# Performance work log

Measured on AMD Instinct MI355X. Metric: run time of the kernel, lower is better.

Reference implementation:

```python
import jax, jax.numpy as jnp
import numpy as np

N, D = 512, 64          # n_objects, object_dim
HG, OG = 256, 256       # g hidden, g output
HF, OF = 256, 64        # f hidden, f output


def setup_inputs() -> dict:
    key = jax.random.key(0)
    ks = jax.random.split(key, 16)
    s = 0.05
    inp = {
        "x": jax.random.normal(ks[0], (N, D), dtype=jnp.float32),
        "q": jax.random.normal(ks[1], (D,), dtype=jnp.float32),
        # MLP g: input 3*D -> HG -> OG (ReLU after every layer, nonlinear=True)
        "g_w1": jax.random.normal(ks[2], (3 * D, HG), dtype=jnp.float32) * s,
        "g_b1": jnp.zeros((HG,), dtype=jnp.float32),
        "g_w2": jax.random.normal(ks[3], (HG, OG), dtype=jnp.float32) * s,
        "g_b2": jnp.zeros((OG,), dtype=jnp.float32),
        # query_expand: D -> HG -> OG (nonlinear=True)
        "qe_w1": jax.random.normal(ks[4], (D, HG), dtype=jnp.float32) * s,
        "qe_b1": jnp.zeros((HG,), dtype=jnp.float32),
        "qe_w2": jax.random.normal(ks[5], (HG, OG), dtype=jnp.float32) * s,
        "qe_b2": jnp.zeros((OG,), dtype=jnp.float32),
        # MLP f: OG -> HF -> OF (ReLU on hidden only, nonlinear=False)
        "f_w1": jax.random.normal(ks[6], (OG, HF), dtype=jnp.float32) * s,
        "f_b1": jnp.zeros((HF,), dtype=jnp.float32),
        "f_w2": jax.random.normal(ks[7], (HF, OF), dtype=jnp.float32) * s,
        "f_b2": jnp.zeros((OF,), dtype=jnp.float32),
    }
    return inp


def reference(x, q, g_w1, g_b1, g_w2, g_b2, qe_w1, qe_b1, qe_w2, qe_b2,
              f_w1, f_b1, f_w2, f_b2):
    n, d = x.shape
    # pair (a,b): first half x_i = x[b], second half x_j = x[a], then query q
    xi = jnp.broadcast_to(x[None, :, :], (n, n, d))   # repeats x along dim 0
    xj = jnp.broadcast_to(x[:, None, :], (n, n, d))   # repeats x along dim 1
    qb = jnp.broadcast_to(q[None, None, :], (n, n, d))
    pair_concat = jnp.concatenate([xi, xj, qb], axis=-1).reshape(n * n, 3 * d)
    # g MLP (ReLU after every layer since nonlinear=True)
    h = jax.nn.relu(pair_concat @ g_w1 + g_b1)
    relations = jax.nn.relu(h @ g_w2 + g_b2)          # [N*N, OG]
    # attentional weighting
    qh = jax.nn.relu(q @ qe_w1 + qe_b1)
    q_exp = jax.nn.relu(qh @ qe_w2 + qe_b2)           # [OG]
    c = jax.nn.softmax(relations @ q_exp, axis=0)     # [N*N]
    embedding = jnp.sum(relations * c[:, None], axis=0)  # [OG]
    # f MLP (no final nonlinearity)
    fh = jax.nn.relu(embedding @ f_w1 + f_b1)
    out = fh @ f_w2 + f_b2                            # [OF]
    return out
```

## Files before the change

kernel.cpp:

```cpp
#include <hip/hip_runtime.h>
#include <hip/hip_bf16.h>

typedef __attribute__((ext_vector_type(8))) short s16x8;
typedef __attribute__((ext_vector_type(4))) float f32x4;

#define NSLOT 128

__device__ __forceinline__ short f2bf(float f) {
    union { float f; unsigned u; } c; c.f = f;
    unsigned u = c.u;
    return (short)((u + 0x7fffu + ((u >> 16) & 1u)) >> 16);
}

__global__ __launch_bounds__(256) void rn_k1(
    const float* __restrict__ x, const float* __restrict__ q,
    const float* __restrict__ g_w1, const float* __restrict__ g_b1,
    const float* __restrict__ g_w2,
    const float* __restrict__ qe_w1, const float* __restrict__ qe_b1,
    const float* __restrict__ qe_w2, const float* __restrict__ qe_b2,
    float* __restrict__ U, float* __restrict__ V,
    float* __restrict__ c0, float* __restrict__ qexp,
    short* __restrict__ w2s, float* __restrict__ accb)
{
    const int blk = blockIdx.x, t = threadIdx.x;

    if (blk < 64) {
        __shared__ float xs[1024];
        const int rg = blk >> 1, half = blk & 1;
        const int r0 = rg << 4;
        #pragma unroll
        for (int i = 0; i < 4; ++i) {
            int idx = i * 256 + t;
            xs[idx] = x[(r0 << 6) + idx];
        }
        float w[64];
        #pragma unroll
        for (int k = 0; k < 64; ++k)
            w[k] = g_w1[(half * 64 + k) * 256 + t];
        __syncthreads();
        float* dst = half ? V : U;
        #pragma unroll 2
        for (int r = 0; r < 16; ++r) {
            float a0 = 0.f, a1 = 0.f, a2 = 0.f, a3 = 0.f;
            #pragma unroll
            for (int k = 0; k < 64; k += 4) {
                const float4 xv = *(const float4*)&xs[r * 64 + k];
                a0 += xv.x * w[k + 0];
                a1 += xv.y * w[k + 1];
                a2 += xv.z * w[k + 2];
                a3 += xv.w * w[k + 3];
            }
            dst[(r0 + r) * 256 + t] = (a0 + a1) + (a2 + a3);
        }
    } else if (blk == 64) {
        __shared__ float sbuf[64];
        __shared__ float qh[256];
        if (t < 64) sbuf[t] = q[t];
        __syncthreads();
        float cc = g_b1[t], hh = qe_b1[t];
        #pragma unroll 4
        for (int k = 0; k < 64; ++k) {
            float qv = sbuf[k];
            cc += qv * g_w1[(128 + k) * 256 + t];
            hh += qv * qe_w1[k * 256 + t];
        }
        c0[t] = cc;
        qh[t] = fmaxf(hh, 0.f);
        __syncthreads();
        float qe = qe_b2[t];
        #pragma unroll 4
        for (int k = 0; k < 256; ++k) qe += qh[k] * qe_w2[k * 256 + t];
        qexp[t] = fmaxf(qe, 0.f);
    } else if (blk < 97) {
        const int S0 = (blk - 65) * 2048 + t * 8;
        const float4 wA = *(const float4*)&g_w2[S0];
        const float4 wB = *(const float4*)&g_w2[S0 + 4];
        float wv8[8] = {wA.x, wA.y, wA.z, wA.w, wB.x, wB.y, wB.z, wB.w};
        #pragma unroll
        for (int i = 0; i < 8; ++i) {
            const int S = S0 + i;
            const int k = S >> 8, col = S & 255;
            const int wv = col >> 6, n = (col >> 4) & 3, l15 = col & 15;
            const int kk = k >> 5, g = (k >> 3) & 3, e = k & 7;
            const int lane = g * 16 + l15;
            w2s[((((wv * 8 + kk) * 4 + n) * 64 + lane) << 3) + e] = f2bf(wv8[i]);
        }
    } else {
        const int total = NSLOT * 257;
        int off = (blk - 97) * 2048 + t * 8;
        #pragma unroll
        for (int i = 0; i < 8; ++i)
            if (off + i < total) accb[off + i] = 0.f;
    }
}

__global__ __launch_bounds__(256, 4) void rn_k2(
    const float* __restrict__ U, const float* __restrict__ V,
    const float* __restrict__ c0, const float* __restrict__ qexp,
    const short* __restrict__ w2s, const float* __restrict__ g_b2,
    float* __restrict__ accb)
{
    __shared__ short hT[64][264];
    __shared__ float srowT[64][4];

    const int bid = blockIdx.x;
    const int a   = bid >> 3;
    const int b0  = (bid & 7) << 6;
    const int tid = threadIdx.x;
    const int wave = tid >> 6, lane = tid & 63;
    const int l15 = lane & 15, g = lane >> 4;
    const int col0 = wave << 6;

    {
        const int c4 = tid & 63;
        const int r0 = tid >> 6;
        const float4 vv  = *(const float4*)&V[a * 256 + c4 * 4];
        const float4 cc  = *(const float4*)&c0[c4 * 4];
        const float4 vcv = make_float4(vv.x + cc.x, vv.y + cc.y,
                                       vv.z + cc.z, vv.w + cc.w);
        #pragma unroll
        for (int it = 0; it < 16; ++it) {
            int row = r0 + it * 4;
            float4 uu = *(const float4*)&U[(b0 + row) * 256 + c4 * 4];
            __hip_bfloat162 p0 = __float22bfloat162_rn(
                make_float2(fmaxf(uu.x + vcv.x, 0.f), fmaxf(uu.y + vcv.y, 0.f)));
            __hip_bfloat162 p1 = __float22bfloat162_rn(
                make_float2(fmaxf(uu.z + vcv.z, 0.f), fmaxf(uu.w + vcv.w, 0.f)));
            uint2 st;
            st.x = *reinterpret_cast<unsigned*>(&p0);
            st.y = *reinterpret_cast<unsigned*>(&p1);
            *reinterpret_cast<uint2*>(&hT[row][c4 * 4]) = st;
        }
    }

    float qe[4], b2c[4];
    #pragma unroll
    for (int n = 0; n < 4; ++n) {
        int col = col0 + n * 16 + l15;
        qe[n]  = qexp[col];
        b2c[n] = g_b2[col];
    }
    __syncthreads();

    f32x4 acc[4][4];
    #pragma unroll
    for (int m = 0; m < 4; ++m)
        #pragma unroll
        for (int n = 0; n < 4; ++n)
            acc[m][n] = (f32x4){b2c[n], b2c[n], b2c[n], b2c[n]};

    #pragma unroll
    for (int kk = 0; kk < 8; ++kk) {
        const int koff = kk * 32 + g * 8;
        s16x8 bfr[4];
        #pragma unroll
        for (int n = 0; n < 4; ++n)
            bfr[n] = *(const s16x8*)&w2s[((wave << 14) + (((kk * 4 + n) << 9))) + (lane << 3)];
        s16x8 afr[4];
        #pragma unroll
        for (int m = 0; m < 4; ++m)
            afr[m] = *(const s16x8*)&hT[m * 16 + l15][koff];
        #pragma unroll
        for (int m = 0; m < 4; ++m)
            #pragma unroll
            for (int n = 0; n < 4; ++n)
                acc[m][n] = __builtin_amdgcn_mfma_f32_16x16x32_bf16(
                    afr[m], bfr[n], acc[m][n], 0, 0, 0);
    }

    #pragma unroll
    for (int m = 0; m < 4; ++m)
        #pragma unroll
        for (int n = 0; n < 4; ++n)
            #pragma unroll
            for (int j = 0; j < 4; ++j)
                acc[m][n][j] = fmaxf(acc[m][n][j], 0.f);

    #pragma unroll
    for (int m = 0; m < 4; ++m) {
        #pragma unroll
        for (int j = 0; j < 4; ++j) {
            float sp = 0.f;
            #pragma unroll
            for (int n = 0; n < 4; ++n) sp += acc[m][n][j] * qe[n];
            sp += __shfl_xor(sp, 1);
            sp += __shfl_xor(sp, 2);
            sp += __shfl_xor(sp, 4);
            sp += __shfl_xor(sp, 8);
            if (l15 == 0) srowT[m * 16 + g * 4 + j][wave] = sp;
        }
    }
    __syncthreads();

    float wrow[4][4];
    #pragma unroll
    for (int m = 0; m < 4; ++m)
        #pragma unroll
        for (int j = 0; j < 4; ++j) {
            const float4 s4 = *(const float4*)&srowT[m * 16 + g * 4 + j][0];
            wrow[m][j] = __expf(s4.x + s4.y + s4.z + s4.w);
        }

    const int slot = bid & (NSLOT - 1);
    if (wave == 0) {
        float ls = 0.f;
        #pragma unroll
        for (int m = 0; m < 4; ++m)
            #pragma unroll
            for (int j = 0; j < 4; ++j) ls += wrow[m][j];
        ls += __shfl_xor(ls, 16);
        ls += __shfl_xor(ls, 32);
        if (lane == 0) atomicAdd(&accb[slot * 257 + 256], ls);
    }

    #pragma unroll
    for (int n = 0; n < 4; ++n) {
        float wv = 0.f;
        #pragma unroll
        for (int m = 0; m < 4; ++m)
            #pragma unroll
            for (int j = 0; j < 4; ++j)
                wv += wrow[m][j] * acc[m][n][j];
        wv += __shfl_xor(wv, 16);
        wv += __shfl_xor(wv, 32);
        if (lane < 16) atomicAdd(&accb[slot * 257 + col0 + n * 16 + lane], wv);
    }
}

__global__ __launch_bounds__(1024) void rn_k4(
    const float* __restrict__ accb,
    const float* __restrict__ f_w1, const float* __restrict__ f_b1,
    const float* __restrict__ f_w2, const float* __restrict__ f_b2,
    float* __restrict__ out)
{
    __shared__ float part[4][256];
    __shared__ float emb[256];
    __shared__ float fh[256];
    __shared__ float lsa[128];
    const int t   = threadIdx.x;
    const int col = t & 255;
    const int sl  = t >> 8;

    float v = 0.f;
    #pragma unroll 8
    for (int s = sl; s < NSLOT; s += 4) v += accb[s * 257 + col];
    part[sl][col] = v;
    if (t < 128) lsa[t] = accb[t * 257 + 256];
    __syncthreads();

    if (sl == 0) {
        float ls = 0.f;
        #pragma unroll 8
        for (int s = 0; s < 128; ++s) ls += lsa[s];
        emb[col] = (part[0][col] + part[1][col] + part[2][col] + part[3][col]) / ls;
    }
    __syncthreads();

    {
        float h = 0.f;
        const int k0 = sl << 6;
        #pragma unroll 8
        for (int k = 0; k < 64; ++k)
            h += emb[k0 + k] * f_w1[(k0 + k) * 256 + col];
        part[sl][col] = h;
    }
    __syncthreads();
    if (sl == 0)
        fh[col] = fmaxf(part[0][col] + part[1][col] + part[2][col] + part[3][col]
                        + f_b1[col], 0.f);
    __syncthreads();

    if (t < 256) {
        const int oc = t & 63, ks = t >> 6;
        float o = 0.f;
        const int k0 = ks << 6;
        #pragma unroll 8
        for (int k = 0; k < 64; ++k)
            o += fh[k0 + k] * f_w2[(k0 + k) * 64 + oc];
        part[ks][oc] = o;
    }
    __syncthreads();
    if (t < 64)
        out[t] = part[0][t] + part[1][t] + part[2][t] + part[3][t] + f_b2[t];
}

extern "C" void kernel_launch(void* const* d_in, const int* in_sizes, int n_in,
                              void* d_out, int out_size, void* d_ws, size_t ws_size,
                              hipStream_t stream) {
    const float* x     = (const float*)d_in[0];
    const float* q     = (const float*)d_in[1];
    const float* g_w1  = (const float*)d_in[2];
    const float* g_b1  = (const float*)d_in[3];
    const float* g_w2  = (const float*)d_in[4];
    const float* g_b2  = (const float*)d_in[5];
    const float* qe_w1 = (const float*)d_in[6];
    const float* qe_b1 = (const float*)d_in[7];
    const float* qe_w2 = (const float*)d_in[8];
    const float* qe_b2 = (const float*)d_in[9];
    const float* f_w1  = (const float*)d_in[10];
    const float* f_b1  = (const float*)d_in[11];
    const float* f_w2  = (const float*)d_in[12];
    const float* f_b2  = (const float*)d_in[13];

    float* wsf  = (float*)d_ws;
    float* U    = wsf;
    float* V    = wsf + 131072;
    float* c0   = wsf + 262144;
    float* qexp = wsf + 262400;
    short* w2s  = (short*)(wsf + 262656);
    float* accb = wsf + 295424;

    hipLaunchKernelGGL(rn_k1, dim3(114), dim3(256), 0, stream,
                       x, q, g_w1, g_b1, g_w2, qe_w1, qe_b1, qe_w2, qe_b2,
                       U, V, c0, qexp, w2s, accb);
    hipLaunchKernelGGL(rn_k2, dim3(4096), dim3(256), 0, stream,
                       U, V, c0, qexp, (const short*)w2s, g_b2, accb);
    hipLaunchKernelGGL(rn_k4, dim3(1), dim3(1024), 0, stream,
                       accb, f_w1, f_b1, f_w2, f_b2, (float*)d_out);
}
```

Baseline: 72.59 us.

## Process four row tiles per block in rn_k2 with persistent loop

rn_k2 now launches 1024 blocks, and each block loops over four 64-row tiles instead of handling a single tile. The loop reuses the V+c0 vector, qexp and bias registers, and builds the next tile's hidden activations in LDS while the softmax weighting of the current tile runs. It also replaces the shuffle row reductions with DPP row sums, uses exp2 for the exponential, raises MFMA priority with setprio, and lowers the occupancy hint to 3. The aim is to cut per-block setup and launch overhead, at the cost of fewer blocks for parallelism and extra synchronization per tile.

Result: slower. 176.2 us (+142.8%).

```diff
diff --git a/kernel.cpp b/kernel.cpp
--- a/kernel.cpp
+++ b/kernel.cpp
@@ -10,6 +10,19 @@
     union { float f; unsigned u; } c; c.f = f;
     unsigned u = c.u;
     return (short)((u + 0x7fffu + ((u >> 16) & 1u)) >> 16);
+}
+__device__ __forceinline__ unsigned pk2(float lo, float hi) {
+    __hip_bfloat162 p = __float22bfloat162_rn(make_float2(lo, hi));
+    return *reinterpret_cast<unsigned*>(&p);
+}
+__device__ __forceinline__ float rowsum16(float x) {
+    union { float f; int i; } a, b;
+    a.f = x;
+    b.i = __builtin_amdgcn_mov_dpp(a.i, 0x121, 0xf, 0xf, true); a.f += b.f;
+    b.i = __builtin_amdgcn_mov_dpp(a.i, 0x122, 0xf, 0xf, true); a.f += b.f;
+    b.i = __builtin_amdgcn_mov_dpp(a.i, 0x124, 0xf, 0xf, true); a.f += b.f;
+    b.i = __builtin_amdgcn_mov_dpp(a.i, 0x128, 0xf, 0xf, true); a.f += b.f;
+    return a.f;
 }
 
 __global__ __launch_bounds__(256) void rn_k1(
@@ -94,7 +107,7 @@
     }
 }
 
-__global__ __launch_bounds__(256, 4) void rn_k2(
+__global__ __launch_bounds__(256, 3) void rn_k2(
     const float* __restrict__ U, const float* __restrict__ V,
     const float* __restrict__ c0, const float* __restrict__ qexp,
     const short* __restrict__ w2s, const float* __restrict__ g_b2,
@@ -103,35 +116,16 @@
     __shared__ short hT[64][264];
     __shared__ float srowT[64][4];
 
-    const int bid = blockIdx.x;
-    const int a   = bid >> 3;
-    const int b0  = (bid & 7) << 6;
-    const int tid = threadIdx.x;
-    const int wave = tid >> 6, lane = tid & 63;
-    const int l15 = lane & 15, g = lane >> 4;
-    const int col0 = wave << 6;
-
-    {
-        const int c4 = tid & 63;
-        const int r0 = tid >> 6;
-        const float4 vv  = *(const float4*)&V[a * 256 + c4 * 4];
-        const float4 cc  = *(const float4*)&c0[c4 * 4];
-        const float4 vcv = make_float4(vv.x + cc.x, vv.y + cc.y,
-                                       vv.z + cc.z, vv.w + cc.w);
-        #pragma unroll
-        for (int it = 0; it < 16; ++it) {
-            int row = r0 + it * 4;
-            float4 uu = *(const float4*)&U[(b0 + row) * 256 + c4 * 4];
-            __hip_bfloat162 p0 = __float22bfloat162_rn(
-                make_float2(fmaxf(uu.x + vcv.x, 0.f), fmaxf(uu.y + vcv.y, 0.f)));
-            __hip_bfloat162 p1 = __float22bfloat162_rn(
-                make_float2(fmaxf(uu.z + vcv.z, 0.f), fmaxf(uu.w + vcv.w, 0.f)));
-            uint2 st;
-            st.x = *reinterpret_cast<unsigned*>(&p0);
-            st.y = *reinterpret_cast<unsigned*>(&p1);
-            *reinterpret_cast<uint2*>(&hT[row][c4 * 4]) = st;
-        }
-    }
+    const int bid   = blockIdx.x;
+    const int a     = bid >> 1;
+    const int bbase = (bid & 1) << 8;
+    const int tid   = threadIdx.x;
+    const int wave  = tid >> 6, lane = tid & 63;
+    const int l15   = lane & 15, g = lane >> 4;
+    const int col0  = wave << 6;
+
+    const int c4 = tid & 63;
+    const int r0 = tid >> 6;
 
     float qe[4], b2c[4];
     #pragma unroll
@@ -140,91 +134,115 @@
         qe[n]  = qexp[col];
         b2c[n] = g_b2[col];
     }
-    __syncthreads();
-
-    f32x4 acc[4][4];
-    #pragma unroll
-    for (int m = 0; m < 4; ++m)
-        #pragma unroll
-        for (int n = 0; n < 4; ++n)
-            acc[m][n] = (f32x4){b2c[n], b2c[n], b2c[n], b2c[n]};
-
-    #pragma unroll
-    for (int kk = 0; kk < 8; ++kk) {
-        const int koff = kk * 32 + g * 8;
-        s16x8 bfr[4];
-        #pragma unroll
-        for (int n = 0; n < 4; ++n)
-            bfr[n] = *(const s16x8*)&w2s[((wave << 14) + (((kk * 4 + n) << 9))) + (lane << 3)];
-        s16x8 afr[4];
+    float4 vcv;
+    {
+        const float4 vv = *(const float4*)&V[a * 256 + c4 * 4];
+        const float4 cc = *(const float4*)&c0[c4 * 4];
+        vcv = make_float4(vv.x + cc.x, vv.y + cc.y, vv.z + cc.z, vv.w + cc.w);
+    }
+
+#define BUILD(B0) { \
+    _Pragma("unroll") \
+    for (int it = 0; it < 16; ++it) { \
+        const int row = r0 + it * 4; \
+        const float4 uu = *(const float4*)&U[((B0) + row) * 256 + c4 * 4]; \
+        uint2 st; \
+        st.x = pk2(fmaxf(uu.x + vcv.x, 0.f), fmaxf(uu.y + vcv.y, 0.f)); \
+        st.y = pk2(fmaxf(uu.z + vcv.z, 0.f), fmaxf(uu.w + vcv.w, 0.f)); \
+        *reinterpret_cast<uint2*>(&hT[row][c4 * 4]) = st; \
+    } }
+
+    BUILD(bbase);
+
+    for (int u = 0; u < 4; ++u) {
+        __syncthreads();
+
+        f32x4 acc[4][4];
         #pragma unroll
         for (int m = 0; m < 4; ++m)
-            afr[m] = *(const s16x8*)&hT[m * 16 + l15][koff];
+            #pragma unroll
+            for (int n = 0; n < 4; ++n)
+                acc[m][n] = (f32x4){b2c[n], b2c[n], b2c[n], b2c[n]};
+
+        #pragma unroll
+        for (int kk = 0; kk < 8; ++kk) {
+            const int koff = kk * 32 + g * 8;
+            s16x8 bfr[4];
+            #pragma unroll
+            for (int n = 0; n < 4; ++n)
+                bfr[n] = *(const s16x8*)&w2s[(wave << 14) + ((kk * 4 + n) << 9) + (lane << 3)];
+            s16x8 afr[4];
+            #pragma unroll
+            for (int m = 0; m < 4; ++m)
+                afr[m] = *(const s16x8*)&hT[m * 16 + l15][koff];
+            __builtin_amdgcn_s_setprio(1);
+            #pragma unroll
+            for (int m = 0; m < 4; ++m)
+                #pragma unroll
+                for (int n = 0; n < 4; ++n)
+                    acc[m][n] = __builtin_amdgcn_mfma_f32_16x16x32_bf16(
+                        afr[m], bfr[n], acc[m][n], 0, 0, 0);
+            __builtin_amdgcn_s_setprio(0);
+        }
+
         #pragma unroll
         for (int m = 0; m < 4; ++m)
             #pragma unroll
             for (int n = 0; n < 4; ++n)
-                acc[m][n] = __builtin_amdgcn_mfma_f32_16x16x32_bf16(
-                    afr[m], bfr[n], acc[m][n], 0, 0, 0);
-    }
-
-    #pragma unroll
-    for (int m = 0; m < 4; ++m)
-        #pragma unroll
-        for (int n = 0; n < 4; ++n)
-            #pragma unroll
-            for (int j = 0; j < 4; ++j)
-                acc[m][n][j] = fmaxf(acc[m][n][j], 0.f);
-
-    #pragma unroll
-    for (int m = 0; m < 4; ++m) {
-        #pragma unroll
-        for (int j = 0; j < 4; ++j) {
-            float sp = 0.f;
-            #pragma unroll
-            for (int n = 0; n < 4; ++n) sp += acc[m][n][j] * qe[n];
-            sp += __shfl_xor(sp, 1);
-            sp += __shfl_xor(sp, 2);
-            sp += __shfl_xor(sp, 4);
-            sp += __shfl_xor(sp, 8);
-            if (l15 == 0) srowT[m * 16 + g * 4 + j][wave] = sp;
-        }
-    }
-    __syncthreads();
-
-    float wrow[4][4];
-    #pragma unroll
-    for (int m = 0; m < 4; ++m)
-        #pragma unroll
-        for (int j = 0; j < 4; ++j) {
-            const float4 s4 = *(const float4*)&srowT[m * 16 + g * 4 + j][0];
-            wrow[m][j] = __expf(s4.x + s4.y + s4.z + s4.w);
-        }
-
-    const int slot = bid & (NSLOT - 1);
-    if (wave == 0) {
-        float ls = 0.f;
+                #pragma unroll
+                for (int j = 0; j < 4; ++j)
+                    acc[m][n][j] = fmaxf(acc[m][n][j], 0.f);
+
+        #pragma unroll
+        for (int m = 0; m < 4; ++m) {
+            #pragma unroll
+            for (int j = 0; j < 4; ++j) {
+                float sp = acc[m][0][j] * qe[0] + acc[m][1][j] * qe[1]
+                         + acc[m][2][j] * qe[2] + acc[m][3][j] * qe[3];
+                sp = rowsum16(sp);
+                if (l15 == 0) srowT[m * 16 + g * 4 + j][wave] = sp;
+            }
+        }
+        __syncthreads();
+
+        if (u < 3) BUILD(bbase + (u + 1) * 64);
+
+        float wrow[4][4];
         #pragma unroll
         for (int m = 0; m < 4; ++m)
             #pragma unroll
-            for (int j = 0; j < 4; ++j) ls += wrow[m][j];
-        ls += __shfl_xor(ls, 16);
-        ls += __shfl_xor(ls, 32);
-        if (lane == 0) atomicAdd(&accb[slot * 257 + 256], ls);
-    }
-
-    #pragma unroll
-    for (int n = 0; n < 4; ++n) {
-        float wv = 0.f;
-        #pragma unroll
-        for (int m = 0; m < 4; ++m)
-            #pragma unroll
-            for (int j = 0; j < 4; ++j)
-                wv += wrow[m][j] * acc[m][n][j];
-        wv += __shfl_xor(wv, 16);
-        wv += __shfl_xor(wv, 32);
-        if (lane < 16) atomicAdd(&accb[slot * 257 + col0 + n * 16 + lane], wv);
-    }
+            for (int j = 0; j < 4; ++j) {
+                const float4 s4 = *(const float4*)&srowT[m * 16 + g * 4 + j][0];
+                wrow[m][j] = __builtin_amdgcn_exp2f(
+                    (s4.x + s4.y + s4.z + s4.w) * 1.4426950408889634f);
+            }
+
+        const int slot = ((bid << 2) | u) & (NSLOT - 1);
+        if (wave == 0) {
+            float ls = 0.f;
+            #pragma unroll
+            for (int m = 0; m < 4; ++m)
+                #pragma unroll
+                for (int j = 0; j < 4; ++j) ls += wrow[m][j];
+            ls += __shfl_xor(ls, 16);
+            ls += __shfl_xor(ls, 32);
+            if (lane == 0) atomicAdd(&accb[slot * 257 + 256], ls);
+        }
+
+        #pragma unroll
+        for (int n = 0; n < 4; ++n) {
+            float wv = 0.f;
+            #pragma unroll
+            for (int m = 0; m < 4; ++m)
+                #pragma unroll
+                for (int j = 0; j < 4; ++j)
+                    wv += wrow[m][j] * acc[m][n][j];
+            wv += __shfl_xor(wv, 16);
+            wv += __shfl_xor(wv, 32);
+            if (lane < 16) atomicAdd(&accb[slot * 257 + col0 + n * 16 + lane], wv);
+        }
+    }
+#undef BUILD
 }
 
 __global__ __launch_bounds__(1024) void rn_k4(
@@ -313,7 +331,7 @@
     hipLaunchKernelGGL(rn_k1, dim3(114), dim3(256), 0, stream,
                        x, q, g_w1, g_b1, g_w2, qe_w1, qe_b1, qe_w2, qe_b2,
                        U, V, c0, qexp, w2s, accb);
-    hipLaunchKernelGGL(rn_k2, dim3(4096), dim3(256), 0, stream,
+    hipLaunchKernelGGL(rn_k2, dim3(1024), dim3(256), 0, stream,
                        U, V, c0, qexp, (const short*)w2s, g_b2, accb);
     hipLaunchKernelGGL(rn_k4, dim3(1), dim3(1024), 0, stream,
                        accb, f_w1, f_b1, f_w2, f_b2, (float*)d_out);
```
